# Performance work log

Hardware: AMD Instinct MI355X
Metric: run time of the kernel (lower is better)

## Reference

```python
import jax, jax.numpy as jnp
import numpy as np

N, F, C, H, E, NC = 100000, 128, 64, 4, 1600000, 2
BN_EPS = 1e-5


def _bn(x, g, b):
    mu = x.mean(0)
    var = x.var(0)  # biased variance, as torch BN uses for normalization
    return (x - mu) / jnp.sqrt(var + BN_EPS) * g + b


def _gat(x, src, dst, W, a_src, a_dst, bias, heads, out_ch, concat, n):
    # x:[n,in] -> h:[n,heads,out_ch]
    h = (x @ W).reshape(n, heads, out_ch)
    e_src = (h * a_src[None]).sum(-1)  # [n,heads]
    e_dst = (h * a_dst[None]).sum(-1)
    logits = jax.nn.leaky_relu(e_src[src] + e_dst[dst], 0.2)  # [e,heads]
    m = jax.ops.segment_max(logits, dst, num_segments=n)
    m = jnp.where(jnp.isfinite(m), m, 0.0)
    ex = jnp.exp(logits - m[dst])
    denom = jax.ops.segment_sum(ex, dst, num_segments=n)
    alpha = ex / denom[dst]  # segment softmax over incoming edges
    out = jax.ops.segment_sum(alpha[:, :, None] * h[src], dst, num_segments=n)
    out = out.reshape(n, heads * out_ch) if concat else out.mean(axis=1)
    return out + bias


def _sage(x, src, dst, Wl, bl, Wr, n):
    agg = jax.ops.segment_sum(x[src], dst, num_segments=n)
    cnt = jax.ops.segment_sum(jnp.ones_like(src, dtype=x.dtype), dst, num_segments=n)
    agg = agg / jnp.maximum(cnt, 1.0)[:, None]  # mean aggregation
    return agg @ Wl + bl + x @ Wr


def setup_inputs() -> dict:
    key = jax.random.key(0)
    ks = jax.random.split(key, 24)
    def rn(k, shape, fan):
        return jax.random.normal(k, shape, jnp.float32) * (1.0 / np.sqrt(fan))
    inp = {}
    inp['x'] = jax.random.normal(ks[0], (N, F), jnp.float32)
    inp['edge_index'] = jax.random.randint(ks[1], (2, E), 0, N, jnp.int32)
    # GAT layer 1: in=F, out=C, heads=H, concat
    inp['W1g'] = rn(ks[2], (F, H * C), F)
    inp['a_src1'] = rn(ks[3], (H, C), C)
    inp['a_dst1'] = rn(ks[4], (H, C), C)
    inp['b1g'] = jnp.zeros((H * C,), jnp.float32)
    inp['bn1g_g'] = jnp.ones((H * C,), jnp.float32)
    inp['bn1g_b'] = jnp.zeros((H * C,), jnp.float32)
    # GAT layer 2: in=H*C, out=C, heads=1, no concat
    inp['W2g'] = rn(ks[5], (H * C, C), H * C)
    inp['a_src2'] = rn(ks[6], (1, C), C)
    inp['a_dst2'] = rn(ks[7], (1, C), C)
    inp['b2g'] = jnp.zeros((C,), jnp.float32)
    # SAGE layer 1
    inp['Wl1'] = rn(ks[8], (F, C), F)
    inp['bl1'] = jnp.zeros((C,), jnp.float32)
    inp['Wr1'] = rn(ks[9], (F, C), F)
    inp['bn1s_g'] = jnp.ones((C,), jnp.float32)
    inp['bn1s_b'] = jnp.zeros((C,), jnp.float32)
    # SAGE layer 2
    inp['Wl2'] = rn(ks[10], (C, C), C)
    inp['bl2'] = jnp.zeros((C,), jnp.float32)
    inp['Wr2'] = rn(ks[11], (C, C), C)
    # fusion MLP
    inp['Wf1'] = rn(ks[12], (2 * C, C), 2 * C)
    inp['bf1'] = jnp.zeros((C,), jnp.float32)
    inp['Wf2'] = rn(ks[13], (C, NC), C)
    inp['bf2'] = jnp.zeros((NC,), jnp.float32)
    return inp


def reference(x, edge_index, W1g, a_src1, a_dst1, b1g, bn1g_g, bn1g_b,
              W2g, a_src2, a_dst2, b2g, Wl1, bl1, Wr1, bn1s_g, bn1s_b,
              Wl2, bl2, Wr2, Wf1, bf1, Wf2, bf2):
    n = x.shape[0]
    src, dst = edge_index[0], edge_index[1]
    # PyG GATConv adds self-loops by default
    loop = jnp.arange(n, dtype=src.dtype)
    src_l = jnp.concatenate([src, loop])
    dst_l = jnp.concatenate([dst, loop])

    # GAT branch (dropout = identity in eval)
    g = _gat(x, src_l, dst_l, W1g, a_src1, a_dst1, b1g, H, C, True, n)
    g = jax.nn.elu(_bn(g, bn1g_g, bn1g_b))
    g = _gat(g, src_l, dst_l, W2g, a_src2, a_dst2, b2g, 1, C, False, n)

    # SAGE branch (no self-loops in SAGEConv)
    s = _sage(x, src, dst, Wl1, bl1, Wr1, n)
    s = jax.nn.relu(_bn(s, bn1s_g, bn1s_b))
    s = _sage(s, src, dst, Wl2, bl2, Wr2, n)

    h = jnp.concatenate([g, s], axis=-1)  # [n, 2C]
    h = jax.nn.relu(h @ Wf1 + bf1)
    return h @ Wf2 + bf2  # logits [n, NC]
```

## Files before the change

kernel.cpp:

```cpp
#include <hip/hip_runtime.h>
#include <math.h>


typedef unsigned short u16;
typedef u16 us4 __attribute__((ext_vector_type(4)));
typedef short s8v __attribute__((ext_vector_type(8)));
typedef float f4v __attribute__((ext_vector_type(4)));

__device__ __forceinline__ float b2f(u16 u) {
  union { unsigned int i; float f; } v; v.i = ((unsigned int)u) << 16; return v.f;
}
__device__ __forceinline__ u16 f2b(float f) {
  union { float f; unsigned int i; } v; v.f = f;
  unsigned int u = v.i;
  return (u16)((u + 0x7fffu + ((u >> 16) & 1u)) >> 16);
}

struct WcastDesc { const float* W; u16* Wt; int K; int M; };
struct WcastAll { WcastDesc d[5]; };
__global__ __launch_bounds__(256) void k_wcast_all(WcastAll a) {
  WcastDesc de = a.d[blockIdx.y];
  int n = de.K * de.M;
  int idx = blockIdx.x * blockDim.x + threadIdx.x;
  if (idx >= n) return;
  int c = idx / de.K, k = idx - c * de.K;
  de.Wt[idx] = f2b(de.W[(size_t)k * de.M + c]);
}

__global__ __launch_bounds__(256) void k_combine(const float* __restrict__ Wl2, const float* __restrict__ Wr2,
                                                 const float* __restrict__ bl2, const float* __restrict__ Wf1,
                                                 const float* __restrict__ bf1, u16* __restrict__ Wc1t,
                                                 u16* __restrict__ Wc2t, float* __restrict__ biasC) {
  int idx = blockIdx.x * 256 + threadIdx.x;
  if (idx >= 4096) return;
  int m = idx >> 6, k = idx & 63;
  float s1 = 0.f, s2 = 0.f;
  for (int j = 0; j < 64; ++j) {
    float wf = Wf1[(size_t)(64 + j) * 64 + m];
    s1 += Wl2[k * 64 + j] * wf;
    s2 += Wr2[k * 64 + j] * wf;
  }
  Wc1t[m * 64 + k] = f2b(s1);
  Wc2t[m * 64 + k] = f2b(s2);
  if (k == 0) {
    float b = bf1[m];
    for (int j = 0; j < 64; ++j) b += bl2[j] * Wf1[(size_t)(64 + j) * 64 + m];
    biasC[m] = b;
  }
}

__global__ __launch_bounds__(256) void k_deg(const int* __restrict__ ei, int* __restrict__ deg, int E) {
  int e = blockIdx.x * blockDim.x + threadIdx.x;
  if (e < E) atomicAdd(&deg[ei[E + e]], 1);
}

__global__ __launch_bounds__(256) void k_scan1(const int* __restrict__ deg, int* __restrict__ row_ptr,
                                               int* __restrict__ bsum, int n) {
  __shared__ int sh[256];
  int tid = threadIdx.x;
  int i = blockIdx.x * 256 + tid;
  int v = (i < n) ? deg[i] : 0;
  sh[tid] = v;
  __syncthreads();
  for (int off = 1; off < 256; off <<= 1) {
    int t = (tid >= off) ? sh[tid - off] : 0;
    __syncthreads();
    sh[tid] += t;
    __syncthreads();
  }
  if (i < n) row_ptr[i] = sh[tid] - v;
  if (tid == 255) bsum[blockIdx.x] = sh[255];
}

__global__ __launch_bounds__(1024) void k_scan2(int* __restrict__ bsum, int* __restrict__ total, int nb) {
  __shared__ int sh[1024];
  int tid = threadIdx.x;
  int v = (tid < nb) ? bsum[tid] : 0;
  sh[tid] = v;
  __syncthreads();
  for (int off = 1; off < 1024; off <<= 1) {
    int t = (tid >= off) ? sh[tid - off] : 0;
    __syncthreads();
    sh[tid] += t;
    __syncthreads();
  }
  if (tid < nb) bsum[tid] = sh[tid] - v;
  if (tid == 1023) *total = sh[1023];
}

__global__ __launch_bounds__(256) void k_scan3(int* __restrict__ row_ptr, const int* __restrict__ bsum, int n) {
  int i = blockIdx.x * 256 + threadIdx.x;
  if (i < n) row_ptr[i] += bsum[blockIdx.x];
}

__global__ __launch_bounds__(256) void k_scatter(const int* __restrict__ ei, const int* __restrict__ row_ptr,
                                                 int* __restrict__ cursor, int* __restrict__ csr_src, int E) {
  int e = blockIdx.x * blockDim.x + threadIdx.x;
  if (e < E) {
    int d = ei[E + e];
    int pos = row_ptr[d] + atomicAdd(&cursor[d], 1);
    csr_src[pos] = ei[e];
  }
}

struct Seg6Ptr { const u16* Wt[6]; };
__global__ __launch_bounds__(256) void k_gemm_fused1(const float* __restrict__ X, Seg6Ptr wp,
                                                     u16* __restrict__ h1, u16* __restrict__ xl,
                                                     u16* __restrict__ xr, const float* __restrict__ bl1,
                                                     const float* __restrict__ a_src1, const float* __restrict__ a_dst1,
                                                     float* __restrict__ es1, float* __restrict__ ed1, int Nrows) {
  __shared__ u16 As[64][40];
  __shared__ u16 Bs[6][64][40];
  int row0 = blockIdx.x * 64;
  int tid = threadIdx.x;
  int w = tid >> 6, lane = tid & 63;
  int lr = tid >> 2;
  int lseg = (tid & 3) * 8;
  f4v acc[6][4];
#pragma unroll
  for (int s = 0; s < 6; ++s)
#pragma unroll
    for (int nn = 0; nn < 4; ++nn) acc[s][nn] = (f4v){0.f, 0.f, 0.f, 0.f};
  int ar = (w << 4) + (lane & 15);
  int ak = (lane >> 4) << 3;

  for (int k0 = 0; k0 < 128; k0 += 32) {
    __syncthreads();
    int gr = row0 + lr;
    s8v av = {};
    if (gr < Nrows) {
      float4 lo = *reinterpret_cast<const float4*>(X + (size_t)gr * 128 + k0 + lseg);
      float4 hi = *reinterpret_cast<const float4*>(X + (size_t)gr * 128 + k0 + lseg + 4);
      av[0] = (short)f2b(lo.x); av[1] = (short)f2b(lo.y); av[2] = (short)f2b(lo.z); av[3] = (short)f2b(lo.w);
      av[4] = (short)f2b(hi.x); av[5] = (short)f2b(hi.y); av[6] = (short)f2b(hi.z); av[7] = (short)f2b(hi.w);
    }
    *reinterpret_cast<s8v*>(&As[lr][lseg]) = av;
#pragma unroll
    for (int s = 0; s < 6; ++s) {
      s8v bv = *reinterpret_cast<const s8v*>(wp.Wt[s] + (size_t)lr * 128 + k0 + lseg);
      *reinterpret_cast<s8v*>(&Bs[s][lr][lseg]) = bv;
    }
    __syncthreads();
    s8v af = *reinterpret_cast<const s8v*>(&As[ar][ak]);
#pragma unroll
    for (int s = 0; s < 6; ++s) {
#pragma unroll
      for (int nn = 0; nn < 4; ++nn) {
        s8v bf = *reinterpret_cast<const s8v*>(&Bs[s][(nn << 4) + (lane & 15)][ak]);
        acc[s][nn] = __builtin_amdgcn_mfma_f32_16x16x32_bf16(af, bf, acc[s][nn], 0, 0, 0);
      }
    }
  }

  int r0 = row0 + (w << 4) + ((lane >> 4) << 2);
  int cc = lane & 15;
#pragma unroll
  for (int s = 0; s < 4; ++s) {
    float pe[4] = {0.f, 0.f, 0.f, 0.f}, pd[4] = {0.f, 0.f, 0.f, 0.f};
#pragma unroll
    for (int nn = 0; nn < 4; ++nn) {
      int col = (nn << 4) + cc;
      float asv = a_src1[s * 64 + col];
      float adv = a_dst1[s * 64 + col];
#pragma unroll
      for (int j = 0; j < 4; ++j) {
        float hv = acc[s][nn][j];
        pe[j] += hv * asv;
        pd[j] += hv * adv;
        int gr = r0 + j;
        if (gr < Nrows) h1[(size_t)gr * 256 + s * 64 + col] = f2b(hv);
      }
    }
#pragma unroll
    for (int off = 1; off < 16; off <<= 1) {
#pragma unroll
      for (int j = 0; j < 4; ++j) {
        pe[j] += __shfl_xor(pe[j], off, 64);
        pd[j] += __shfl_xor(pd[j], off, 64);
      }
    }
    if (cc == 0) {
#pragma unroll
      for (int j = 0; j < 4; ++j) {
        int gr = r0 + j;
        if (gr < Nrows) {
          es1[(size_t)gr * 4 + s] = pe[j];
          ed1[(size_t)gr * 4 + s] = pd[j];
        }
      }
    }
  }
#pragma unroll
  for (int nn = 0; nn < 4; ++nn) {
    int gc = (nn << 4) + cc;
    float bv = bl1[gc];
#pragma unroll
    for (int j = 0; j < 4; ++j) {
      int gr = r0 + j;
      if (gr < Nrows) {
        xl[(size_t)gr * 64 + gc] = f2b(acc[4][nn][j]);
        xr[(size_t)gr * 64 + gc] = f2b(acc[5][nn][j] + bv);
      }
    }
  }
}

__global__ __launch_bounds__(256) void k_gemm_bn(const u16* __restrict__ A, const u16* __restrict__ Wt,
                                                 const float* __restrict__ sc, const float* __restrict__ sh,
                                                 const float* __restrict__ a_src2, const float* __restrict__ a_dst2,
                                                 u16* __restrict__ C, float* __restrict__ es2,
                                                 float* __restrict__ ed2, int Nrows) {
  __shared__ u16 As[64][40];
  __shared__ u16 Bs[64][40];
  int row0 = blockIdx.x * 64;
  int tid = threadIdx.x;
  int w = tid >> 6, lane = tid & 63;
  int lr = tid >> 2;
  int lseg = (tid & 3) * 8;
  f4v acc[4];
#pragma unroll
  for (int nn = 0; nn < 4; ++nn) acc[nn] = (f4v){0.f, 0.f, 0.f, 0.f};
  int ar = (w << 4) + (lane & 15);
  int ak = (lane >> 4) << 3;

  for (int k0 = 0; k0 < 256; k0 += 32) {
    __syncthreads();
    int gr = row0 + lr;
    s8v av = {};
    if (gr < Nrows) {
      av = *reinterpret_cast<const s8v*>(A + (size_t)gr * 256 + k0 + lseg);
#pragma unroll
      for (int j = 0; j < 8; ++j) {
        int c = k0 + lseg + j;
        float a = b2f((u16)av[j]) * sc[c] + sh[c];
        a = (a > 0.f) ? a : (__expf(a) - 1.f);
        av[j] = (short)f2b(a);
      }
    }
    *reinterpret_cast<s8v*>(&As[lr][lseg]) = av;
    s8v bv = *reinterpret_cast<const s8v*>(Wt + (size_t)lr * 256 + k0 + lseg);
    *reinterpret_cast<s8v*>(&Bs[lr][lseg]) = bv;
    __syncthreads();
    s8v af = *reinterpret_cast<const s8v*>(&As[ar][ak]);
#pragma unroll
    for (int nn = 0; nn < 4; ++nn) {
      s8v bf = *reinterpret_cast<const s8v*>(&Bs[(nn << 4) + (lane & 15)][ak]);
      acc[nn] = __builtin_amdgcn_mfma_f32_16x16x32_bf16(af, bf, acc[nn], 0, 0, 0);
    }
  }
  int r0 = row0 + (w << 4) + ((lane >> 4) << 2);
  int cc = lane & 15;
  float pe[4] = {0.f, 0.f, 0.f, 0.f}, pd[4] = {0.f, 0.f, 0.f, 0.f};
#pragma unroll
  for (int nn = 0; nn < 4; ++nn) {
    int gc = (nn << 4) + cc;
    float asv = a_src2[gc], adv = a_dst2[gc];
#pragma unroll
    for (int j = 0; j < 4; ++j) {
      float hv = acc[nn][j];
      pe[j] += hv * asv;
      pd[j] += hv * adv;
      int gr = r0 + j;
      if (gr < Nrows) C[(size_t)gr * 64 + gc] = f2b(hv);
    }
  }
#pragma unroll
  for (int off = 1; off < 16; off <<= 1) {
#pragma unroll
    for (int j = 0; j < 4; ++j) {
      pe[j] += __shfl_xor(pe[j], off, 64);
      pd[j] += __shfl_xor(pd[j], off, 64);
    }
  }
  if (cc == 0) {
#pragma unroll
    for (int j = 0; j < 4; ++j) {
      int gr = r0 + j;
      if (gr < Nrows) { es2[gr] = pe[j]; ed2[gr] = pd[j]; }
    }
  }
}

template <int H>
__global__ __launch_bounds__(256) void k_gat_fused(const u16* __restrict__ h, const float* __restrict__ es,
                                                   const float* __restrict__ ed, const int* __restrict__ row_ptr,
                                                   const int* __restrict__ csr, const float* __restrict__ bias,
                                                   u16* __restrict__ out, int n) {
  constexpr int HC = H * 64;
  constexpr int VW = HC / 64;
  constexpr int SL = 64 / H;
  constexpr int CAP = 256;
  __shared__ float lal[4][CAP * H];
  int widx = threadIdx.x >> 6;
  int wid = blockIdx.x * 4 + widx;
  int lane = threadIdx.x & 63;
  float* A = lal[widx];
  bool active = wid < n;
  int start = 0, deg = 0;
  if (active) { start = row_ptr[wid]; deg = row_ptr[wid + 1] - start; }
  int ne = deg + 1;

  int hh = lane % H;
  int esl = lane / H;
  float m = -1e30f, s = 0.f;
  if (active) {
    float edst = ed[(size_t)wid * H + hh];
    for (int e = esl; e < ne; e += SL) {
      int sn = (e < deg) ? csr[start + e] : wid;
      float v = es[(size_t)sn * H + hh] + edst;
      v = (v >= 0.f) ? v : 0.2f * v;
      if (e < CAP) A[e * H + hh] = v;
      if (v > m) { s = s * __expf(m - v) + 1.f; m = v; }
      else s += __expf(v - m);
    }
  }
#pragma unroll
  for (int off = H; off < 64; off <<= 1) {
    float mo = __shfl_xor(m, off, 64);
    float so = __shfl_xor(s, off, 64);
    float M = fmaxf(m, mo);
    s = s * __expf(m - M) + so * __expf(mo - M);
    m = M;
  }
  float invS = 1.f / s;
  if (active) {
    int lim = (ne < CAP) ? ne : CAP;
    for (int e = esl; e < lim; e += SL) A[e * H + hh] = __expf(A[e * H + hh] - m) * invS;
  }
  __syncthreads();

  if (active) {
    int c0 = lane * VW;
    int hl = c0 >> 6;
    float mh = __shfl(m, hl, 64);
    float iSh = __shfl(invS, hl, 64);
    float edl = 0.f;
    if (ne > CAP) edl = ed[(size_t)wid * H + hl];
    float acc[VW] = {};
    {
      float aS;
      if (deg < CAP) aS = A[deg * H + hl];
      else {
        float v = es[(size_t)wid * H + hl] + edl;
        v = (v >= 0.f) ? v : 0.2f * v;
        aS = __expf(v - mh) * iSh;
      }
      if constexpr (VW == 4) {
        us4 hv = *(reinterpret_cast<const us4*>(h + (size_t)wid * HC) + lane);
#pragma unroll
        for (int j = 0; j < 4; ++j) acc[j] = aS * b2f(hv[j]);
      } else {
        acc[0] = aS * b2f(h[(size_t)wid * HC + lane]);
      }
    }
    int e = 0;
    for (; e + 4 <= deg; e += 4) {
      int sn[4];
      float al[4];
#pragma unroll
      for (int i = 0; i < 4; ++i) {
        sn[i] = csr[start + e + i];
        if (e + i < CAP) al[i] = A[(e + i) * H + hl];
        else {
          float v = es[(size_t)sn[i] * H + hl] + edl;
          v = (v >= 0.f) ? v : 0.2f * v;
          al[i] = __expf(v - mh) * iSh;
        }
      }
#pragma unroll
      for (int i = 0; i < 4; ++i) {
        if constexpr (VW == 4) {
          us4 hv = *(reinterpret_cast<const us4*>(h + (size_t)sn[i] * HC) + lane);
#pragma unroll
          for (int j = 0; j < 4; ++j) acc[j] += al[i] * b2f(hv[j]);
        } else {
          acc[0] += al[i] * b2f(h[(size_t)sn[i] * HC + lane]);
        }
      }
    }
    for (; e < deg; ++e) {
      int sn = csr[start + e];
      float al;
      if (e < CAP) al = A[e * H + hl];
      else {
        float v = es[(size_t)sn * H + hl] + edl;
        v = (v >= 0.f) ? v : 0.2f * v;
        al = __expf(v - mh) * iSh;
      }
      if constexpr (VW == 4) {
        us4 hv = *(reinterpret_cast<const us4*>(h + (size_t)sn * HC) + lane);
#pragma unroll
        for (int j = 0; j < 4; ++j) acc[j] += al * b2f(hv[j]);
      } else {
        acc[0] += al * b2f(h[(size_t)sn * HC + lane]);
      }
    }
#pragma unroll
    for (int j = 0; j < VW; ++j) out[(size_t)wid * HC + c0 + j] = f2b(acc[j] + bias[c0 + j]);
  }
}

__global__ __launch_bounds__(256) void k_sage_agg64(const u16* __restrict__ x, const int* __restrict__ row_ptr,
                                                    const int* __restrict__ csr, const u16* __restrict__ Cin,
                                                    const float* __restrict__ sc, const float* __restrict__ sh,
                                                    u16* __restrict__ agg, int n) {
  int wid = (blockIdx.x * blockDim.x + threadIdx.x) >> 6;
  int lane = threadIdx.x & 63;
  if (wid >= n) return;
  int start = row_ptr[wid];
  int deg = row_ptr[wid + 1] - start;
  bool bn = sc != nullptr;
  float scv = 1.f, shv = 0.f;
  if (bn) { scv = sc[lane]; shv = sh[lane]; }
  float acc = 0.f;
  int e = 0;
  for (; e + 4 <= deg; e += 4) {
    int sn[4];
#pragma unroll
    for (int i = 0; i < 4; ++i) sn[i] = csr[start + e + i];
#pragma unroll
    for (int i = 0; i < 4; ++i) {
      float v = b2f(x[(size_t)sn[i] * 64 + lane]);
      if (bn) v = fmaxf(v * scv + shv, 0.f);
      acc += v;
    }
  }
  for (; e < deg; ++e) {
    float v = b2f(x[(size_t)csr[start + e] * 64 + lane]);
    if (bn) v = fmaxf(v * scv + shv, 0.f);
    acc += v;
  }
  float inv = 1.f / fmaxf((float)deg, 1.f);
  float base = Cin ? b2f(Cin[(size_t)wid * 64 + lane]) : 0.f;
  agg[(size_t)wid * 64 + lane] = f2b(acc * inv + base);
}

template <int CH>
__global__ __launch_bounds__(256) void k_bn_stats(const u16* __restrict__ x, float* __restrict__ stats, int n) {
  constexpr int RPB = 256 / CH;
  int tid = threadIdx.x;
  int c = tid % CH;
  int rsub = tid / CH;
  float s = 0.f, q = 0.f;
  for (int r = blockIdx.x * RPB + rsub; r < n; r += gridDim.x * RPB) {
    float v = b2f(x[(size_t)r * CH + c]);
    s += v;
    q += v * v;
  }
  __shared__ float ls[256], lq[256];
  ls[tid] = s; lq[tid] = q;
  __syncthreads();
  if (tid < CH) {
#pragma unroll
    for (int i = 1; i < RPB; ++i) { s += ls[tid + i * CH]; q += lq[tid + i * CH]; }
    atomicAdd(&stats[c], s);
    atomicAdd(&stats[CH + c], q);
  }
}

__global__ __launch_bounds__(256) void k_bn_final2(const float* __restrict__ statsG, const float* __restrict__ statsS,
                                                   const float* __restrict__ gG, const float* __restrict__ bG,
                                                   const float* __restrict__ gS, const float* __restrict__ bS,
                                                   float* __restrict__ scG, float* __restrict__ shG,
                                                   float* __restrict__ scS, float* __restrict__ shS, int n) {
  int c = threadIdx.x;
  float invn = 1.f / (float)n;
  {
    float mu = statsG[c] * invn;
    float var = statsG[256 + c] * invn - mu * mu;
    float rs = rsqrtf(var + 1e-5f) * gG[c];
    scG[c] = rs;
    shG[c] = bG[c] - mu * rs;
  }
  if (c < 64) {
    float mu = statsS[c] * invn;
    float var = statsS[64 + c] * invn - mu * mu;
    float rs = rsqrtf(var + 1e-5f) * gS[c];
    scS[c] = rs;
    shS[c] = bS[c] - mu * rs;
  }
}

__global__ __launch_bounds__(256) void k_gemm_final(const u16* __restrict__ A1, const u16* __restrict__ W1,
                                                    const u16* __restrict__ A2, const u16* __restrict__ W2,
                                                    const u16* __restrict__ A3, const u16* __restrict__ W3,
                                                    const float* __restrict__ scS, const float* __restrict__ shS,
                                                    const float* __restrict__ biasC, const float* __restrict__ Wf2,
                                                    const float* __restrict__ bf2, float* __restrict__ out,
                                                    int Nrows) {
  __shared__ u16 As[64][40];
  __shared__ u16 Bs[64][40];
  int row0 = blockIdx.x * 64;
  int tid = threadIdx.x;
  int w = tid >> 6, lane = tid & 63;
  int lr = tid >> 2;
  int lseg = (tid & 3) * 8;
  f4v acc[4];
#pragma unroll
  for (int nn = 0; nn < 4; ++nn) acc[nn] = (f4v){0.f, 0.f, 0.f, 0.f};
  int ar = (w << 4) + (lane & 15);
  int ak = (lane >> 4) << 3;

  const u16* Aarr[3] = {A1, A2, A3};
  const u16* Warr[3] = {W1, W2, W3};
#pragma unroll
  for (int ph = 0; ph < 3; ++ph) {
    const u16* A = Aarr[ph];
    const u16* Wt = Warr[ph];
#pragma unroll
    for (int k0 = 0; k0 < 64; k0 += 32) {
      __syncthreads();
      int gr = row0 + lr;
      s8v av = {};
      if (gr < Nrows) {
        av = *reinterpret_cast<const s8v*>(A + (size_t)gr * 64 + k0 + lseg);
        if (ph == 2) {
#pragma unroll
          for (int j = 0; j < 8; ++j) {
            int c = k0 + lseg + j;
            float a = fmaxf(b2f((u16)av[j]) * scS[c] + shS[c], 0.f);
            av[j] = (short)f2b(a);
          }
        }
      }
      *reinterpret_cast<s8v*>(&As[lr][lseg]) = av;
      s8v bv = *reinterpret_cast<const s8v*>(Wt + (size_t)lr * 64 + k0 + lseg);
      *reinterpret_cast<s8v*>(&Bs[lr][lseg]) = bv;
      __syncthreads();
      s8v af = *reinterpret_cast<const s8v*>(&As[ar][ak]);
#pragma unroll
      for (int nn = 0; nn < 4; ++nn) {
        s8v bf = *reinterpret_cast<const s8v*>(&Bs[(nn << 4) + (lane & 15)][ak]);
        acc[nn] = __builtin_amdgcn_mfma_f32_16x16x32_bf16(af, bf, acc[nn], 0, 0, 0);
      }
    }
  }

  int r0 = row0 + (w << 4) + ((lane >> 4) << 2);
  int cc = lane & 15;
  float p0[4] = {0.f, 0.f, 0.f, 0.f}, p1[4] = {0.f, 0.f, 0.f, 0.f};
#pragma unroll
  for (int nn = 0; nn < 4; ++nn) {
    int col = (nn << 4) + cc;
    float bC = biasC[col];
    float w0 = Wf2[col * 2 + 0], w1 = Wf2[col * 2 + 1];
#pragma unroll
    for (int j = 0; j < 4; ++j) {
      float f = fmaxf(acc[nn][j] + bC, 0.f);
      p0[j] += f * w0;
      p1[j] += f * w1;
    }
  }
#pragma unroll
  for (int off = 1; off < 16; off <<= 1) {
#pragma unroll
    for (int j = 0; j < 4; ++j) {
      p0[j] += __shfl_xor(p0[j], off, 64);
      p1[j] += __shfl_xor(p1[j], off, 64);
    }
  }
  if (cc == 0) {
    float b0 = bf2[0], b1 = bf2[1];
#pragma unroll
    for (int j = 0; j < 4; ++j) {
      int gr = r0 + j;
      if (gr < Nrows) {
        out[(size_t)gr * 2 + 0] = p0[j] + b0;
        out[(size_t)gr * 2 + 1] = p1[j] + b1;
      }
    }
  }
}

extern "C" void kernel_launch(void* const* d_in, const int* in_sizes, int n_in,
                              void* d_out, int out_size, void* d_ws, size_t ws_size,
                              hipStream_t stream) {
  const float* x      = (const float*)d_in[0];
  const int*   ei     = (const int*)d_in[1];
  const float* W1g    = (const float*)d_in[2];
  const float* a_src1 = (const float*)d_in[3];
  const float* a_dst1 = (const float*)d_in[4];
  const float* b1g    = (const float*)d_in[5];
  const float* bn1g_g = (const float*)d_in[6];
  const float* bn1g_b = (const float*)d_in[7];
  const float* W2g    = (const float*)d_in[8];
  const float* a_src2 = (const float*)d_in[9];
  const float* a_dst2 = (const float*)d_in[10];
  const float* b2g    = (const float*)d_in[11];
  const float* Wl1    = (const float*)d_in[12];
  const float* bl1    = (const float*)d_in[13];
  const float* Wr1    = (const float*)d_in[14];
  const float* bn1s_g = (const float*)d_in[15];
  const float* bn1s_b = (const float*)d_in[16];
  const float* Wl2    = (const float*)d_in[17];
  const float* bl2    = (const float*)d_in[18];
  const float* Wr2    = (const float*)d_in[19];
  const float* Wf1    = (const float*)d_in[20];
  const float* bf1    = (const float*)d_in[21];
  const float* Wf2    = (const float*)d_in[22];
  const float* bf2    = (const float*)d_in[23];

  const int N = in_sizes[0] / 128;
  const int E = in_sizes[1] / 2;

  char* ws = (char*)d_ws;
  size_t off = 0;
  auto alloc = [&](size_t bytes) -> void* {
    size_t o = (off + 255) & ~(size_t)255;
    off = o + bytes;
    return (void*)(ws + o);
  };

  u16* h1b   = (u16*)alloc((size_t)N * 256 * 2);
  u16* gb    = (u16*)alloc((size_t)N * 256 * 2);
  u16* h2b   = (u16*)alloc((size_t)N * 64 * 2);
  u16* g2b   = (u16*)alloc((size_t)N * 64 * 2);
  u16* xlb   = (u16*)alloc((size_t)N * 64 * 2);
  u16* xrb   = (u16*)alloc((size_t)N * 64 * 2);
  u16* s1b   = (u16*)alloc((size_t)N * 64 * 2);
  float* es1 = (float*)alloc((size_t)N * 4 * 4);
  float* ed1 = (float*)alloc((size_t)N * 4 * 4);
  float* es2 = (float*)alloc((size_t)N * 4);
  float* ed2 = (float*)alloc((size_t)N * 4);
  int* deg     = (int*)alloc((size_t)N * 2 * 4);
  int* cursor  = deg + N;
  int* row_ptr = (int*)alloc((size_t)(N + 1) * 4);
  int* bsum    = (int*)alloc(1024 * 4);
  int* csr     = (int*)alloc((size_t)E * 4);
  float* statsG = (float*)alloc((512 + 128) * 4);
  float* statsS = statsG + 512;
  float* scg   = (float*)alloc(256 * 4);
  float* shg   = (float*)alloc(256 * 4);
  float* scs   = (float*)alloc(64 * 4);
  float* shs   = (float*)alloc(64 * 4);
  float* biasC = (float*)alloc(64 * 4);
  u16* W1t  = (u16*)alloc(256 * 128 * 2);
  u16* W2t  = (u16*)alloc(64 * 256 * 2);
  u16* Wl1t = (u16*)alloc(64 * 128 * 2);
  u16* Wr1t = (u16*)alloc(64 * 128 * 2);
  u16* Wf1at= (u16*)alloc(64 * 64 * 2);
  u16* Wc1t = (u16*)alloc(64 * 64 * 2);
  u16* Wc2t = (u16*)alloc(64 * 64 * 2);
  u16* sagg2b = h1b;

  const int tb = 256;
  const int nwb = (N + 3) / 4;
  const int nsb = (N + 255) / 256;
  const int gx = (N + 63) / 64;

  hipMemsetAsync(deg, 0, (size_t)N * 2 * 4, stream);
  hipMemsetAsync(statsG, 0, (512 + 128) * 4, stream);
  k_deg<<<(E + tb - 1) / tb, tb, 0, stream>>>(ei, deg, E);
  k_scan1<<<nsb, 256, 0, stream>>>(deg, row_ptr, bsum, N);
  k_scan2<<<1, 1024, 0, stream>>>(bsum, row_ptr + N, nsb);
  k_scan3<<<nsb, 256, 0, stream>>>(row_ptr, bsum, N);
  k_scatter<<<(E + tb - 1) / tb, tb, 0, stream>>>(ei, row_ptr, cursor, csr, E);

  WcastAll wa;
  wa.d[0] = { W1g, W1t, 128, 256 };
  wa.d[1] = { W2g, W2t, 256, 64 };
  wa.d[2] = { Wl1, Wl1t, 128, 64 };
  wa.d[3] = { Wr1, Wr1t, 128, 64 };
  wa.d[4] = { Wf1, Wf1at, 64, 64 };
  dim3 wgrid((128 * 256 + tb - 1) / tb, 5);
  k_wcast_all<<<wgrid, tb, 0, stream>>>(wa);
  k_combine<<<16, 256, 0, stream>>>(Wl2, Wr2, bl2, Wf1, bf1, Wc1t, Wc2t, biasC);

  Seg6Ptr sp;
  sp.Wt[0] = W1t;
  sp.Wt[1] = W1t + 64 * 128;
  sp.Wt[2] = W1t + 128 * 128;
  sp.Wt[3] = W1t + 192 * 128;
  sp.Wt[4] = Wl1t;
  sp.Wt[5] = Wr1t;
  k_gemm_fused1<<<gx, 256, 0, stream>>>(x, sp, h1b, xlb, xrb, bl1, a_src1, a_dst1, es1, ed1, N);

  k_gat_fused<4><<<nwb, 256, 0, stream>>>(h1b, es1, ed1, row_ptr, csr, b1g, gb, N);
  k_bn_stats<256><<<256, 256, 0, stream>>>(gb, statsG, N);

  k_sage_agg64<<<nwb, 256, 0, stream>>>(xlb, row_ptr, csr, xrb, nullptr, nullptr, s1b, N);
  k_bn_stats<64><<<256, 256, 0, stream>>>(s1b, statsS, N);
  k_bn_final2<<<1, 256, 0, stream>>>(statsG, statsS, bn1g_g, bn1g_b, bn1s_g, bn1s_b,
                                     scg, shg, scs, shs, N);

  k_gemm_bn<<<gx, 256, 0, stream>>>(gb, W2t, scg, shg, a_src2, a_dst2, h2b, es2, ed2, N);
  k_gat_fused<1><<<nwb, 256, 0, stream>>>(h2b, es2, ed2, row_ptr, csr, b2g, g2b, N);

  k_sage_agg64<<<nwb, 256, 0, stream>>>(s1b, row_ptr, csr, nullptr, scs, shs, sagg2b, N);

  k_gemm_final<<<gx, 256, 0, stream>>>(g2b, Wf1at, sagg2b, Wc1t, s1b, Wc2t,
                                       scs, shs, biasC, Wf2, bf2, (float*)d_out, N);
}
```

Baseline: 836.1 us.

## Split GAT into per-edge alpha pass and head-major per-head aggregation

Stores the layer-1 GAT features head-major, one [N,64] slab per head, and splits the fused GAT kernel in two. A stats kernel writes the per-edge softmax weights to a global buffer, and a per-head aggregation kernel gathers 128-byte rows instead of 512-byte rows. The input is pre-cast to bf16, and the first GEMM is split across a grid y dimension with one weight segment per block. The gathered working set per pass gets smaller, which should improve cache hit rate. The cost is extra global traffic for the alpha arrays (E*4 floats), a second pass over the CSR, recomputed A-tile loads across 6 blocks, and more kernel launches.

```diff
diff --git a/kernel.cpp b/kernel.cpp
--- a/kernel.cpp
+++ b/kernel.cpp
@@ -14,6 +14,15 @@
   union { float f; unsigned int i; } v; v.f = f;
   unsigned int u = v.i;
   return (u16)((u + 0x7fffu + ((u >> 16) & 1u)) >> 16);
+}
+
+__global__ __launch_bounds__(256) void k_cast(const float* __restrict__ s, u16* __restrict__ d, int n4) {
+  int i = blockIdx.x * blockDim.x + threadIdx.x;
+  if (i < n4) {
+    float4 v = *(reinterpret_cast<const float4*>(s) + i);
+    us4 o = { f2b(v.x), f2b(v.y), f2b(v.z), f2b(v.w) };
+    *(reinterpret_cast<us4*>(d) + i) = o;
+  }
 }
 
 struct WcastDesc { const float* W; u16* Wt; int K; int M; };
@@ -103,24 +112,22 @@
   }
 }
 
-struct Seg6Ptr { const u16* Wt[6]; };
-__global__ __launch_bounds__(256) void k_gemm_fused1(const float* __restrict__ X, Seg6Ptr wp,
-                                                     u16* __restrict__ h1, u16* __restrict__ xl,
-                                                     u16* __restrict__ xr, const float* __restrict__ bl1,
-                                                     const float* __restrict__ a_src1, const float* __restrict__ a_dst1,
-                                                     float* __restrict__ es1, float* __restrict__ ed1, int Nrows) {
+struct Seg { const u16* Wt; u16* out; int ldout; const float* bias; int head; };
+struct Segs6 { Seg s[6]; };
+__global__ __launch_bounds__(256) void k_gemm_multi(const u16* __restrict__ A, Segs6 sg,
+                                                    const float* __restrict__ a_src1, const float* __restrict__ a_dst1,
+                                                    float* __restrict__ es1, float* __restrict__ ed1, int Nrows) {
+  Seg seg = sg.s[blockIdx.y];
   __shared__ u16 As[64][40];
-  __shared__ u16 Bs[6][64][40];
+  __shared__ u16 Bs[64][40];
   int row0 = blockIdx.x * 64;
   int tid = threadIdx.x;
   int w = tid >> 6, lane = tid & 63;
   int lr = tid >> 2;
   int lseg = (tid & 3) * 8;
-  f4v acc[6][4];
-#pragma unroll
-  for (int s = 0; s < 6; ++s)
-#pragma unroll
-    for (int nn = 0; nn < 4; ++nn) acc[s][nn] = (f4v){0.f, 0.f, 0.f, 0.f};
+  f4v acc[4];
+#pragma unroll
+  for (int nn = 0; nn < 4; ++nn) acc[nn] = (f4v){0.f, 0.f, 0.f, 0.f};
   int ar = (w << 4) + (lane & 15);
   int ak = (lane >> 4) << 3;
 
@@ -128,34 +135,32 @@
     __syncthreads();
     int gr = row0 + lr;
     s8v av = {};
-    if (gr < Nrows) {
-      float4 lo = *reinterpret_cast<const float4*>(X + (size_t)gr * 128 + k0 + lseg);
-      float4 hi = *reinterpret_cast<const float4*>(X + (size_t)gr * 128 + k0 + lseg + 4);
-      av[0] = (short)f2b(lo.x); av[1] = (short)f2b(lo.y); av[2] = (short)f2b(lo.z); av[3] = (short)f2b(lo.w);
-      av[4] = (short)f2b(hi.x); av[5] = (short)f2b(hi.y); av[6] = (short)f2b(hi.z); av[7] = (short)f2b(hi.w);
-    }
+    if (gr < Nrows) av = *reinterpret_cast<const s8v*>(A + (size_t)gr * 128 + k0 + lseg);
     *reinterpret_cast<s8v*>(&As[lr][lseg]) = av;
-#pragma unroll
-    for (int s = 0; s < 6; ++s) {
-      s8v bv = *reinterpret_cast<const s8v*>(wp.Wt[s] + (size_t)lr * 128 + k0 + lseg);
-      *reinterpret_cast<s8v*>(&Bs[s][lr][lseg]) = bv;
-    }
+    s8v bv = *reinterpret_cast<const s8v*>(seg.Wt + (size_t)lr * 128 + k0 + lseg);
+    *reinterpret_cast<s8v*>(&Bs[lr][lseg]) = bv;
     __syncthreads();
     s8v af = *reinterpret_cast<const s8v*>(&As[ar][ak]);
 #pragma unroll
-    for (int s = 0; s < 6; ++s) {
-#pragma unroll
-      for (int nn = 0; nn < 4; ++nn) {
-        s8v bf = *reinterpret_cast<const s8v*>(&Bs[s][(nn << 4) + (lane & 15)][ak]);
-        acc[s][nn] = __builtin_amdgcn_mfma_f32_16x16x32_bf16(af, bf, acc[s][nn], 0, 0, 0);
-      }
-    }
-  }
-
+    for (int nn = 0; nn < 4; ++nn) {
+      s8v bf = *reinterpret_cast<const s8v*>(&Bs[(nn << 4) + (lane & 15)][ak]);
+      acc[nn] = __builtin_amdgcn_mfma_f32_16x16x32_bf16(af, bf, acc[nn], 0, 0, 0);
+    }
+  }
   int r0 = row0 + (w << 4) + ((lane >> 4) << 2);
   int cc = lane & 15;
 #pragma unroll
-  for (int s = 0; s < 4; ++s) {
+  for (int nn = 0; nn < 4; ++nn) {
+    int gc = (nn << 4) + cc;
+    float bv = seg.bias ? seg.bias[gc] : 0.f;
+#pragma unroll
+    for (int j = 0; j < 4; ++j) {
+      int gr = r0 + j;
+      if (gr < Nrows) seg.out[(size_t)gr * seg.ldout + gc] = f2b(acc[nn][j] + bv);
+    }
+  }
+  if (seg.head >= 0) {
+    int s = seg.head;
     float pe[4] = {0.f, 0.f, 0.f, 0.f}, pd[4] = {0.f, 0.f, 0.f, 0.f};
 #pragma unroll
     for (int nn = 0; nn < 4; ++nn) {
@@ -164,11 +169,8 @@
       float adv = a_dst1[s * 64 + col];
 #pragma unroll
       for (int j = 0; j < 4; ++j) {
-        float hv = acc[s][nn][j];
-        pe[j] += hv * asv;
-        pd[j] += hv * adv;
-        int gr = r0 + j;
-        if (gr < Nrows) h1[(size_t)gr * 256 + s * 64 + col] = f2b(hv);
+        pe[j] += acc[nn][j] * asv;
+        pd[j] += acc[nn][j] * adv;
       }
     }
 #pragma unroll
@@ -187,19 +189,6 @@
           es1[(size_t)gr * 4 + s] = pe[j];
           ed1[(size_t)gr * 4 + s] = pd[j];
         }
-      }
-    }
-  }
-#pragma unroll
-  for (int nn = 0; nn < 4; ++nn) {
-    int gc = (nn << 4) + cc;
-    float bv = bl1[gc];
-#pragma unroll
-    for (int j = 0; j < 4; ++j) {
-      int gr = r0 + j;
-      if (gr < Nrows) {
-        xl[(size_t)gr * 64 + gc] = f2b(acc[4][nn][j]);
-        xr[(size_t)gr * 64 + gc] = f2b(acc[5][nn][j] + bv);
       }
     }
   }
@@ -281,41 +270,27 @@
   }
 }
 
-template <int H>
-__global__ __launch_bounds__(256) void k_gat_fused(const u16* __restrict__ h, const float* __restrict__ es,
-                                                   const float* __restrict__ ed, const int* __restrict__ row_ptr,
-                                                   const int* __restrict__ csr, const float* __restrict__ bias,
-                                                   u16* __restrict__ out, int n) {
-  constexpr int HC = H * 64;
-  constexpr int VW = HC / 64;
-  constexpr int SL = 64 / H;
-  constexpr int CAP = 256;
-  __shared__ float lal[4][CAP * H];
-  int widx = threadIdx.x >> 6;
-  int wid = blockIdx.x * 4 + widx;
+__global__ __launch_bounds__(256) void k_gat_stats4(const float* __restrict__ es, const float* __restrict__ ed,
+                                                    const int* __restrict__ row_ptr, const int* __restrict__ csr,
+                                                    float* __restrict__ alphaE, float* __restrict__ alphaS, int n) {
+  int wid = (blockIdx.x * blockDim.x + threadIdx.x) >> 6;
   int lane = threadIdx.x & 63;
-  float* A = lal[widx];
-  bool active = wid < n;
-  int start = 0, deg = 0;
-  if (active) { start = row_ptr[wid]; deg = row_ptr[wid + 1] - start; }
-  int ne = deg + 1;
-
-  int hh = lane % H;
-  int esl = lane / H;
+  if (wid >= n) return;
+  int start = row_ptr[wid];
+  int deg = row_ptr[wid + 1] - start;
+  int h = lane & 3, esl = lane >> 2;
+  float edst = ed[(size_t)wid * 4 + h];
+
   float m = -1e30f, s = 0.f;
-  if (active) {
-    float edst = ed[(size_t)wid * H + hh];
-    for (int e = esl; e < ne; e += SL) {
-      int sn = (e < deg) ? csr[start + e] : wid;
-      float v = es[(size_t)sn * H + hh] + edst;
-      v = (v >= 0.f) ? v : 0.2f * v;
-      if (e < CAP) A[e * H + hh] = v;
-      if (v > m) { s = s * __expf(m - v) + 1.f; m = v; }
-      else s += __expf(v - m);
-    }
-  }
-#pragma unroll
-  for (int off = H; off < 64; off <<= 1) {
+  for (int e = esl; e < deg + 1; e += 16) {
+    int sn = (e < deg) ? csr[start + e] : wid;
+    float v = es[(size_t)sn * 4 + h] + edst;
+    v = (v >= 0.f) ? v : 0.2f * v;
+    if (v > m) { s = s * __expf(m - v) + 1.f; m = v; }
+    else s += __expf(v - m);
+  }
+#pragma unroll
+  for (int off = 4; off < 64; off <<= 1) {
     float mo = __shfl_xor(m, off, 64);
     float so = __shfl_xor(s, off, 64);
     float M = fmaxf(m, mo);
@@ -323,81 +298,84 @@
     m = M;
   }
   float invS = 1.f / s;
-  if (active) {
-    int lim = (ne < CAP) ? ne : CAP;
-    for (int e = esl; e < lim; e += SL) A[e * H + hh] = __expf(A[e * H + hh] - m) * invS;
-  }
-  __syncthreads();
-
-  if (active) {
-    int c0 = lane * VW;
-    int hl = c0 >> 6;
-    float mh = __shfl(m, hl, 64);
-    float iSh = __shfl(invS, hl, 64);
-    float edl = 0.f;
-    if (ne > CAP) edl = ed[(size_t)wid * H + hl];
-    float acc[VW] = {};
-    {
-      float aS;
-      if (deg < CAP) aS = A[deg * H + hl];
-      else {
-        float v = es[(size_t)wid * H + hl] + edl;
-        v = (v >= 0.f) ? v : 0.2f * v;
-        aS = __expf(v - mh) * iSh;
-      }
-      if constexpr (VW == 4) {
-        us4 hv = *(reinterpret_cast<const us4*>(h + (size_t)wid * HC) + lane);
-#pragma unroll
-        for (int j = 0; j < 4; ++j) acc[j] = aS * b2f(hv[j]);
-      } else {
-        acc[0] = aS * b2f(h[(size_t)wid * HC + lane]);
-      }
-    }
-    int e = 0;
-    for (; e + 4 <= deg; e += 4) {
-      int sn[4];
-      float al[4];
-#pragma unroll
-      for (int i = 0; i < 4; ++i) {
-        sn[i] = csr[start + e + i];
-        if (e + i < CAP) al[i] = A[(e + i) * H + hl];
-        else {
-          float v = es[(size_t)sn[i] * H + hl] + edl;
-          v = (v >= 0.f) ? v : 0.2f * v;
-          al[i] = __expf(v - mh) * iSh;
-        }
-      }
-#pragma unroll
-      for (int i = 0; i < 4; ++i) {
-        if constexpr (VW == 4) {
-          us4 hv = *(reinterpret_cast<const us4*>(h + (size_t)sn[i] * HC) + lane);
-#pragma unroll
-          for (int j = 0; j < 4; ++j) acc[j] += al[i] * b2f(hv[j]);
-        } else {
-          acc[0] += al[i] * b2f(h[(size_t)sn[i] * HC + lane]);
-        }
-      }
-    }
-    for (; e < deg; ++e) {
-      int sn = csr[start + e];
-      float al;
-      if (e < CAP) al = A[e * H + hl];
-      else {
-        float v = es[(size_t)sn * H + hl] + edl;
-        v = (v >= 0.f) ? v : 0.2f * v;
-        al = __expf(v - mh) * iSh;
-      }
-      if constexpr (VW == 4) {
-        us4 hv = *(reinterpret_cast<const us4*>(h + (size_t)sn * HC) + lane);
-#pragma unroll
-        for (int j = 0; j < 4; ++j) acc[j] += al * b2f(hv[j]);
-      } else {
-        acc[0] += al * b2f(h[(size_t)sn * HC + lane]);
-      }
-    }
-#pragma unroll
-    for (int j = 0; j < VW; ++j) out[(size_t)wid * HC + c0 + j] = f2b(acc[j] + bias[c0 + j]);
-  }
+  for (int e = esl; e < deg + 1; e += 16) {
+    int sn = (e < deg) ? csr[start + e] : wid;
+    float v = es[(size_t)sn * 4 + h] + edst;
+    v = (v >= 0.f) ? v : 0.2f * v;
+    float a = __expf(v - m) * invS;
+    if (e < deg) alphaE[(size_t)(start + e) * 4 + h] = a;
+    else alphaS[(size_t)wid * 4 + h] = a;
+  }
+}
+
+__global__ __launch_bounds__(256) void k_gat_stats1(const float* __restrict__ es, const float* __restrict__ ed,
+                                                    const int* __restrict__ row_ptr, const int* __restrict__ csr,
+                                                    float* __restrict__ alphaE, float* __restrict__ alphaS, int n) {
+  int wid = (blockIdx.x * blockDim.x + threadIdx.x) >> 6;
+  int lane = threadIdx.x & 63;
+  if (wid >= n) return;
+  int start = row_ptr[wid];
+  int deg = row_ptr[wid + 1] - start;
+  float edst = ed[wid];
+  float m = -1e30f, s = 0.f;
+  for (int e = lane; e < deg + 1; e += 64) {
+    int sn = (e < deg) ? csr[start + e] : wid;
+    float v = es[sn] + edst;
+    v = (v >= 0.f) ? v : 0.2f * v;
+    if (v > m) { s = s * __expf(m - v) + 1.f; m = v; }
+    else s += __expf(v - m);
+  }
+#pragma unroll
+  for (int off = 1; off < 64; off <<= 1) {
+    float mo = __shfl_xor(m, off, 64);
+    float so = __shfl_xor(s, off, 64);
+    float M = fmaxf(m, mo);
+    s = s * __expf(m - M) + so * __expf(mo - M);
+    m = M;
+  }
+  float invS = 1.f / s;
+  for (int e = lane; e < deg + 1; e += 64) {
+    int sn = (e < deg) ? csr[start + e] : wid;
+    float v = es[sn] + edst;
+    v = (v >= 0.f) ? v : 0.2f * v;
+    float a = __expf(v - m) * invS;
+    if (e < deg) alphaE[start + e] = a;
+    else alphaS[wid] = a;
+  }
+}
+
+template <int H>
+__global__ __launch_bounds__(256) void k_gat_agg_head(const u16* __restrict__ htab, const float* __restrict__ alphaE,
+                                                      const float* __restrict__ alphaS, const int* __restrict__ row_ptr,
+                                                      const int* __restrict__ csr, const float* __restrict__ bias,
+                                                      u16* __restrict__ out, int n) {
+  int wid = (blockIdx.x * blockDim.x + threadIdx.x) >> 6;
+  int lane = threadIdx.x & 63;
+  int head = blockIdx.y;
+  if (wid >= n) return;
+  const u16* h = htab + (size_t)head * n * 64;
+  int start = row_ptr[wid];
+  int deg = row_ptr[wid + 1] - start;
+
+  float acc = alphaS[(size_t)wid * H + head] * b2f(h[(size_t)wid * 64 + lane]);
+  int e = 0;
+  for (; e + 4 <= deg; e += 4) {
+    int sn[4];
+    float al[4];
+#pragma unroll
+    for (int i = 0; i < 4; ++i) {
+      sn[i] = csr[start + e + i];
+      al[i] = alphaE[(size_t)(start + e + i) * H + head];
+    }
+#pragma unroll
+    for (int i = 0; i < 4; ++i) acc += al[i] * b2f(h[(size_t)sn[i] * 64 + lane]);
+  }
+  for (; e < deg; ++e) {
+    int sn = csr[start + e];
+    float al = alphaE[(size_t)(start + e) * H + head];
+    acc += al * b2f(h[(size_t)sn * 64 + lane]);
+  }
+  out[(size_t)wid * (H * 64) + head * 64 + lane] = f2b(acc + bias[head * 64 + lane]);
 }
 
 __global__ __launch_bounds__(256) void k_sage_agg64(const u16* __restrict__ x, const int* __restrict__ row_ptr,
@@ -611,6 +589,7 @@
     return (void*)(ws + o);
   };
 
+  u16* xb    = (u16*)alloc((size_t)N * 128 * 2);
   u16* h1b   = (u16*)alloc((size_t)N * 256 * 2);
   u16* gb    = (u16*)alloc((size_t)N * 256 * 2);
   u16* h2b   = (u16*)alloc((size_t)N * 64 * 2);
@@ -622,6 +601,8 @@
   float* ed1 = (float*)alloc((size_t)N * 4 * 4);
   float* es2 = (float*)alloc((size_t)N * 4);
   float* ed2 = (float*)alloc((size_t)N * 4);
+  float* alphaE = (float*)alloc((size_t)E * 4 * 4);
+  float* alphaS = (float*)alloc((size_t)N * 4 * 4);
   int* deg     = (int*)alloc((size_t)N * 2 * 4);
   int* cursor  = deg + N;
   int* row_ptr = (int*)alloc((size_t)(N + 1) * 4);
@@ -656,6 +637,7 @@
   k_scan3<<<nsb, 256, 0, stream>>>(row_ptr, bsum, N);
   k_scatter<<<(E + tb - 1) / tb, tb, 0, stream>>>(ei, row_ptr, cursor, csr, E);
 
+  k_cast<<<((N * 128 / 4) + tb - 1) / tb, tb, 0, stream>>>(x, xb, N * 128 / 4);
   WcastAll wa;
   wa.d[0] = { W1g, W1t, 128, 256 };
   wa.d[1] = { W2g, W2t, 256, 64 };
@@ -666,16 +648,17 @@
   k_wcast_all<<<wgrid, tb, 0, stream>>>(wa);
   k_combine<<<16, 256, 0, stream>>>(Wl2, Wr2, bl2, Wf1, bf1, Wc1t, Wc2t, biasC);
 
-  Seg6Ptr sp;
-  sp.Wt[0] = W1t;
-  sp.Wt[1] = W1t + 64 * 128;
-  sp.Wt[2] = W1t + 128 * 128;
-  sp.Wt[3] = W1t + 192 * 128;
-  sp.Wt[4] = Wl1t;
-  sp.Wt[5] = Wr1t;
-  k_gemm_fused1<<<gx, 256, 0, stream>>>(x, sp, h1b, xlb, xrb, bl1, a_src1, a_dst1, es1, ed1, N);
-
-  k_gat_fused<4><<<nwb, 256, 0, stream>>>(h1b, es1, ed1, row_ptr, csr, b1g, gb, N);
+  Segs6 sg;
+  sg.s[0] = { W1t,             h1b + (size_t)0 * N * 64, 64, nullptr, 0 };
+  sg.s[1] = { W1t + 64 * 128,  h1b + (size_t)1 * N * 64, 64, nullptr, 1 };
+  sg.s[2] = { W1t + 128 * 128, h1b + (size_t)2 * N * 64, 64, nullptr, 2 };
+  sg.s[3] = { W1t + 192 * 128, h1b + (size_t)3 * N * 64, 64, nullptr, 3 };
+  sg.s[4] = { Wl1t,            xlb, 64, nullptr, -1 };
+  sg.s[5] = { Wr1t,            xrb, 64, bl1,     -1 };
+  k_gemm_multi<<<dim3(gx, 6), 256, 0, stream>>>(xb, sg, a_src1, a_dst1, es1, ed1, N);
+
+  k_gat_stats4<<<nwb, 256, 0, stream>>>(es1, ed1, row_ptr, csr, alphaE, alphaS, N);
+  k_gat_agg_head<4><<<dim3(nwb, 4), 256, 0, stream>>>(h1b, alphaE, alphaS, row_ptr, csr, b1g, gb, N);
   k_bn_stats<256><<<256, 256, 0, stream>>>(gb, statsG, N);
 
   k_sage_agg64<<<nwb, 256, 0, stream>>>(xlb, row_ptr, csr, xrb, nullptr, nullptr, s1b, N);
@@ -684,7 +667,8 @@
                                      scg, shg, scs, shs, N);
 
   k_gemm_bn<<<gx, 256, 0, stream>>>(gb, W2t, scg, shg, a_src2, a_dst2, h2b, es2, ed2, N);
-  k_gat_fused<1><<<nwb, 256, 0, stream>>>(h2b, es2, ed2, row_ptr, csr, b2g, g2b, N);
+  k_gat_stats1<<<nwb, 256, 0, stream>>>(es2, ed2, row_ptr, csr, alphaE, alphaS, N);
+  k_gat_agg_head<1><<<dim3(nwb, 1), 256, 0, stream>>>(h2b, alphaE, alphaS, row_ptr, csr, b2g, g2b, N);
 
   k_sage_agg64<<<nwb, 256, 0, stream>>>(s1b, row_ptr, csr, nullptr, scs, shs, sagg2b, N);
 
```

Result: slower. 932.7 us (+11.6%).
